# Kernel tuning notes

Hardware: AMD Instinct MI355X
Metric: run time of the kernel (lower is better)

Reference implementation:

```python
import jax, jax.numpy as jnp
import numpy as np

B, C, H, W = 256, 768, 14, 14
S = 196  # sample_size
HID = 512
OUT = 2


def setup_inputs() -> dict:
    key = jax.random.key(0)
    ks = jax.random.split(key, 10)
    x = jax.random.normal(ks[0], (B, C, H, W), dtype=jnp.float32)
    pxs = jax.random.randint(ks[1], (B, S, 2), 0, H, dtype=jnp.int32)
    pys = jax.random.randint(ks[2], (B, S, 2), 0, H, dtype=jnp.int32)
    scale = 0.02
    W1 = jax.random.normal(ks[3], (2 * C, HID), dtype=jnp.float32) * scale
    b1 = jnp.zeros((HID,), dtype=jnp.float32)
    W2 = jax.random.normal(ks[4], (HID, HID), dtype=jnp.float32) * scale
    b2 = jnp.zeros((HID,), dtype=jnp.float32)
    W3 = jax.random.normal(ks[5], (HID, OUT), dtype=jnp.float32) * scale
    b3 = jnp.zeros((OUT,), dtype=jnp.float32)
    return {"x": x, "W1": W1, "b1": b1, "W2": W2, "b2": b2,
            "W3": W3, "b3": b3, "pxs": pxs, "pys": pys}


def _gather_pts(x_flat, pxy):
    # x_flat: [B, C, H*W]; pxy: [B, S, 2] -> [B, S, C]
    idx = pxy[:, :, 0] * W + pxy[:, :, 1]            # [B, S]
    g = jnp.take_along_axis(x_flat, idx[:, None, :].astype(jnp.int32), axis=2)  # [B, C, S]
    return g.transpose(0, 2, 1)                       # [B, S, C]


def reference(x, W1, b1, W2, b2, W3, b3, pxs, pys):
    x_flat = x.reshape(B, C, H * W)
    ptsx = _gather_pts(x_flat, pxs)                   # [B, S, C]
    ptsy = _gather_pts(x_flat, pys)                   # [B, S, C]
    feats = jnp.concatenate([ptsx, ptsy], axis=2)     # [B, S, 2C]
    h = jax.nn.relu(feats @ W1 + b1)
    h = jax.nn.relu(h @ W2 + b2)
    pred = h @ W3 + b3                                # [B, S, 2]
    predxy = pred.reshape(-1, OUT)                    # [B*S, 2]
    # use_abs=False, normalize=False: deltaxy = (pxs - pys) + (H - 1)
    deltaxy = (pxs - pys).astype(jnp.float32).reshape(-1, 2) + (H - 1)
    return predxy, deltaxy
```

## Files before the change

kernel.cpp:

```cpp
#include <hip/hip_runtime.h>
#include <hip/hip_bf16.h>

typedef __attribute__((ext_vector_type(4))) float f32x4;
typedef __attribute__((ext_vector_type(4))) int   int4v;
typedef __attribute__((ext_vector_type(8))) int   int8v;

__device__ __forceinline__ unsigned char f2fp8(float f) {
    unsigned char s = (__float_as_uint(f) >> 24) & 0x80;
    float a = fabsf(f);
    if (a >= 448.f) return s | 0x7E;
    if (a < 0.015625f) {
        int q = (int)(a * 512.0f + 0.5f);
        return s | (unsigned char)q;
    }
    unsigned int u = __float_as_uint(a);
    u += 0x0007FFFF + ((u >> 20) & 1);
    int e8 = (int)((u >> 23) & 0xFF) - 120;
    if (e8 >= 16) return s | 0x7E;
    return s | (unsigned char)((e8 << 3) | ((u >> 20) & 7));
}
__device__ __forceinline__ void gload_lds16(const void* g, void* l) {
    __builtin_amdgcn_global_load_lds((const __attribute__((address_space(1))) void*)g,
                                     (__attribute__((address_space(3))) void*)l, 16, 0, 0);
}

#define BATCH 256
#define CHAN  768
#define HW    196
#define SPS   196
#define HID   512
#define MROWS 50176
#define K1    1536
#define WSCL  64.0f
#define WINV  0.015625f
#define SC1   0x7F7F7F7F


__global__ void transpose_cast_fp8(const float* __restrict__ in, unsigned char* __restrict__ out,
                                   int K, int N) {
    int idx = blockIdx.x * 256 + threadIdx.x;
    if (idx >= K * N) return;
    int n = idx / K, k = idx - n * K;
    out[idx] = f2fp8(in[(size_t)k * N + n] * WSCL);
}

__global__ __launch_bounds__(256) void gather_feats(const float* __restrict__ x,
                                                    const int* __restrict__ pxs,
                                                    const int* __restrict__ pys,
                                                    unsigned char* __restrict__ feats,
                                                    float* __restrict__ out) {
    __shared__ float lds[64 * 197];
    int chunk = blockIdx.x;
    int b     = blockIdx.y;
    int c0 = chunk * 64;
    const float* xb = x + ((size_t)b * CHAN + c0) * HW;
    for (int t = threadIdx.x; t < 64 * HW; t += 256) {
        int j = t / HW, p = t - j * HW;
        lds[j * 197 + p] = xb[t];
    }
    if (chunk == 0) {
        for (int i = threadIdx.x; i < SPS * 2; i += 256) {
            int idx = b * SPS * 2 + i;
            out[MROWS * 2 + idx] = (float)(pxs[idx] - pys[idx]) + 13.0f;
        }
    }
    __syncthreads();
    int wid = threadIdx.x >> 6, lane = threadIdx.x & 63;
    int g = lane >> 4;
    int cq = (lane & 15) * 4;
    for (int sb = wid * 4; sb < SPS; sb += 16) {
        int s = sb + g;
        int base = (b * SPS + s) * 2;
        int ix = pxs[base] * 14 + pxs[base + 1];
        int iy = pys[base] * 14 + pys[base + 1];
        const float* lx = lds + cq * 197;
        unsigned int ux = 0, uy = 0;
        ux = __builtin_amdgcn_cvt_pk_fp8_f32(lx[ix],       lx[197 + ix], ux, false);
        ux = __builtin_amdgcn_cvt_pk_fp8_f32(lx[394 + ix], lx[591 + ix], ux, true);
        uy = __builtin_amdgcn_cvt_pk_fp8_f32(lx[iy],       lx[197 + iy], uy, false);
        uy = __builtin_amdgcn_cvt_pk_fp8_f32(lx[394 + iy], lx[591 + iy], uy, true);
        size_t ro = (size_t)(b * SPS + s) * K1;
        *(unsigned int*)(feats + ro + c0 + cq)        = ux;
        *(unsigned int*)(feats + ro + CHAN + c0 + cq) = uy;
    }
}

__global__ __launch_bounds__(512, 1)
void mlp_fused(const unsigned char* __restrict__ feats,
               const unsigned char* __restrict__ W1t,
               const float* __restrict__ b1,
               const unsigned char* __restrict__ W2t,
               const float* __restrict__ b2,
               const float* __restrict__ W3,
               const float* __restrict__ b3,
               float* __restrict__ out) {
    extern __shared__ char smem[];
    const int t = threadIdx.x;
    const int wid = t >> 6, lane = t & 63;
    const int lr = lane & 15, lk = lane >> 4;
    const int mBase = blockIdx.x * 64;
    f32x4 acc[4][4] = {};

    auto stage1 = [&](int buf, int kt) {
        char* Ab = smem + buf * 8192;
        char* Bb = smem + 16384 + buf * 65536;
        {
            int row = t >> 3, cs = (t & 7) ^ (row & 7);
            gload_lds16(feats + (size_t)(mBase + row) * K1 + kt * 128 + cs * 16,
                        Ab + t * 16);
        }
        #pragma unroll
        for (int i = 0; i < 8; ++i) {
            int lin = i * 512 + t, row = lin >> 3, cs = (lin & 7) ^ (row & 7);
            gload_lds16(W1t + (size_t)row * K1 + kt * 128 + cs * 16,
                        Bb + lin * 16);
        }
    };
    auto frag128 = [&](const char* rowp, int r) -> int8v {
        union { int4v h[2]; int8v v; } u;
        u.h[0] = *(const int4v*)(rowp + (((2 * lk + 0) ^ (r & 7)) * 16));
        u.h[1] = *(const int4v*)(rowp + (((2 * lk + 1) ^ (r & 7)) * 16));
        return u.v;
    };
    auto compute1 = [&](int buf) {
        const char* Ab = smem + buf * 8192;
        const char* Bb = smem + 16384 + buf * 65536;
        int8v af[4];
        #pragma unroll
        for (int m = 0; m < 4; ++m) {
            int r = m * 16 + lr;
            af[m] = frag128(Ab + r * 128, r);
        }
        #pragma unroll
        for (int n = 0; n < 4; ++n) {
            int r = wid * 64 + n * 16 + lr;
            int8v bf = frag128(Bb + r * 128, r);
            #pragma unroll
            for (int m = 0; m < 4; ++m)
                acc[m][n] = __builtin_amdgcn_mfma_scale_f32_16x16x128_f8f6f4(
                    af[m], bf, acc[m][n], 0, 0, 0, SC1, 0, SC1);
        }
    };

    stage1(0, 0);
    __syncthreads();
    int cur = 0;
    for (int kt = 0; kt < 12; ++kt) {
        if (kt + 1 < 12) stage1(cur ^ 1, kt + 1);
        compute1(cur);
        __syncthreads();
        cur ^= 1;
    }

    char* h1l = smem + 16384;
    float* red = (float*)smem;
    #pragma unroll
    for (int n = 0; n < 4; ++n) {
        int c = wid * 64 + n * 16 + lr;
        int c16 = wid * 4 + n;
        float bv = b1[c];
        #pragma unroll
        for (int m = 0; m < 4; ++m) {
            int r0 = m * 16 + lk * 4;
            float v0 = fmaxf(acc[m][n][0] * WINV + bv, 0.f);
            float v1 = fmaxf(acc[m][n][1] * WINV + bv, 0.f);
            float v2 = fmaxf(acc[m][n][2] * WINV + bv, 0.f);
            float v3 = fmaxf(acc[m][n][3] * WINV + bv, 0.f);
            unsigned int u = __builtin_amdgcn_cvt_pk_fp8_f32(v0, v1, 0u, false);
            u = __builtin_amdgcn_cvt_pk_fp8_f32(v2, v3, u, true);
            #pragma unroll
            for (int j = 0; j < 4; ++j) {
                int r = r0 + j;
                h1l[r * 512 + ((c16 ^ (r & 31)) * 16) + lr] =
                    (unsigned char)((u >> (8 * j)) & 0xff);
            }
        }
    }
    __syncthreads();

    auto frag512 = [&](int r, int kt2) -> int8v {
        int g = kt2 * 8 + lk * 2;
        union { int4v h[2]; int8v v; } u;
        u.h[0] = *(const int4v*)(h1l + r * 512 + (((g + 0) ^ (r & 31)) * 16));
        u.h[1] = *(const int4v*)(h1l + r * 512 + (((g + 1) ^ (r & 31)) * 16));
        return u.v;
    };
    #pragma unroll
    for (int p2 = 0; p2 < 2; ++p2) {
        int8v b2f[2][4];
        float bv2[2], w30[2], w31[2];
        #pragma unroll
        for (int n2 = 0; n2 < 2; ++n2) {
            int c2 = wid * 64 + p2 * 32 + n2 * 16 + lr;
            const unsigned char* rp = W2t + (size_t)c2 * 512;
            #pragma unroll
            for (int kt2 = 0; kt2 < 4; ++kt2)
                b2f[n2][kt2] = *(const int8v*)(rp + kt2 * 128 + lk * 32);
            bv2[n2] = b2[c2];
            w30[n2] = W3[c2 * 2];
            w31[n2] = W3[c2 * 2 + 1];
        }
        #pragma unroll
        for (int s = 0; s < 4; ++s) {
            f32x4 acc2[2] = {};
            #pragma unroll
            for (int kt2 = 0; kt2 < 4; ++kt2) {
                int8v a2 = frag512(s * 16 + lr, kt2);
                acc2[0] = __builtin_amdgcn_mfma_scale_f32_16x16x128_f8f6f4(
                    a2, b2f[0][kt2], acc2[0], 0, 0, 0, SC1, 0, SC1);
                acc2[1] = __builtin_amdgcn_mfma_scale_f32_16x16x128_f8f6f4(
                    a2, b2f[1][kt2], acc2[1], 0, 0, 0, SC1, 0, SC1);
            }
            float p0[4] = {0.f, 0.f, 0.f, 0.f}, p1[4] = {0.f, 0.f, 0.f, 0.f};
            #pragma unroll
            for (int n2 = 0; n2 < 2; ++n2) {
                #pragma unroll
                for (int j = 0; j < 4; ++j) {
                    float v = fmaxf(acc2[n2][j] * WINV + bv2[n2], 0.f);
                    p0[j] += v * w30[n2];
                    p1[j] += v * w31[n2];
                }
            }
            #pragma unroll
            for (int j = 0; j < 4; ++j) {
                #pragma unroll
                for (int msk = 1; msk < 16; msk <<= 1) {
                    p0[j] += __shfl_xor(p0[j], msk);
                    p1[j] += __shfl_xor(p1[j], msk);
                }
                if (lr == 0) {
                    int r = s * 16 + lk * 4 + j;
                    if (p2 == 0) {
                        red[r * 17 + wid * 2 + 0] = p0[j];
                        red[r * 17 + wid * 2 + 1] = p1[j];
                    } else {
                        red[r * 17 + wid * 2 + 0] += p0[j];
                        red[r * 17 + wid * 2 + 1] += p1[j];
                    }
                }
            }
        }
    }
    __syncthreads();

    if (t < 128) {
        int row = t >> 1, comp = t & 1;
        float v = b3[comp];
        #pragma unroll
        for (int w = 0; w < 8; ++w)
            v += red[row * 17 + w * 2 + comp];
        out[(size_t)(mBase + row) * 2 + comp] = v;
    }
}

extern "C" void kernel_launch(void* const* d_in, const int* in_sizes, int n_in,
                              void* d_out, int out_size, void* d_ws, size_t ws_size,
                              hipStream_t stream) {
    const float* x  = (const float*)d_in[0];
    const float* W1 = (const float*)d_in[1];
    const float* b1 = (const float*)d_in[2];
    const float* W2 = (const float*)d_in[3];
    const float* b2 = (const float*)d_in[4];
    const float* W3 = (const float*)d_in[5];
    const float* b3 = (const float*)d_in[6];
    const int*  pxs = (const int*)d_in[7];
    const int*  pys = (const int*)d_in[8];
    float* out = (float*)d_out;
    char* ws = (char*)d_ws;

    unsigned char* W1t   = (unsigned char*)(ws + 0);
    unsigned char* W2t   = (unsigned char*)(ws + 786432);
    unsigned char* feats = (unsigned char*)(ws + 1048576);

    hipFuncSetAttribute((const void*)mlp_fused,
                        hipFuncAttributeMaxDynamicSharedMemorySize, 147456);

    transpose_cast_fp8<<<(K1 * HID + 255) / 256, 256, 0, stream>>>(W1, W1t, K1, HID);
    transpose_cast_fp8<<<(HID * HID + 255) / 256, 256, 0, stream>>>(W2, W2t, HID, HID);
    gather_feats<<<dim3(12, BATCH), 256, 0, stream>>>(x, pxs, pys, feats, out);
    mlp_fused<<<MROWS / 64, 512, 147456, stream>>>(feats, W1t, b1, W2t, b2, W3, b3, out);
}
```

Measured before the change: 179.5 us.

## Gather rows inside GEMM from transposed fp8 x, split N into halves

Stops materialising the per-sample feature matrix. x is instead transposed to a pixel-major fp8 layout, and the GEMM loads A tiles by gathered row index, using precomputed pixel indices. The first GEMM is split into two N-halves, which halves the B staging buffer and shared memory and allows two blocks per CU. The two weight-cast kernels are merged into one launch. The risks are recomputing A loads for each half, more register pressure from holding h1 in registers, and scattered row reads.

```diff
diff --git a/kernel.cpp b/kernel.cpp
--- a/kernel.cpp
+++ b/kernel.cpp
@@ -34,145 +34,178 @@
 #define WSCL  64.0f
 #define WINV  0.015625f
 #define SC1   0x7F7F7F7F
-
-
-__global__ void transpose_cast_fp8(const float* __restrict__ in, unsigned char* __restrict__ out,
-                                   int K, int N) {
+#define GPITCH 198
+
+
+__global__ void prep_weights(const float* __restrict__ W1, const float* __restrict__ W2,
+                             unsigned char* __restrict__ W1t, unsigned char* __restrict__ W2t) {
     int idx = blockIdx.x * 256 + threadIdx.x;
-    if (idx >= K * N) return;
-    int n = idx / K, k = idx - n * K;
-    out[idx] = f2fp8(in[(size_t)k * N + n] * WSCL);
-}
-
-__global__ __launch_bounds__(256) void gather_feats(const float* __restrict__ x,
-                                                    const int* __restrict__ pxs,
-                                                    const int* __restrict__ pys,
-                                                    unsigned char* __restrict__ feats,
-                                                    float* __restrict__ out) {
-    __shared__ float lds[64 * 197];
+    if (idx < K1 * HID) {
+        int n = idx / K1, k = idx - n * K1;
+        W1t[idx] = f2fp8(W1[(size_t)k * HID + n] * WSCL);
+    } else {
+        int i = idx - K1 * HID;
+        int n = i / HID, k = i - n * HID;
+        W2t[i] = f2fp8(W2[(size_t)k * HID + n] * WSCL);
+    }
+}
+
+__global__ __launch_bounds__(512) void xpose8(const float* __restrict__ x,
+                                              const int* __restrict__ pxs,
+                                              const int* __restrict__ pys,
+                                              unsigned char* __restrict__ x8,
+                                              int* __restrict__ pidx,
+                                              float* __restrict__ out) {
+    __shared__ float lds[64 * GPITCH];
     int chunk = blockIdx.x;
     int b     = blockIdx.y;
     int c0 = chunk * 64;
-    const float* xb = x + ((size_t)b * CHAN + c0) * HW;
-    for (int t = threadIdx.x; t < 64 * HW; t += 256) {
-        int j = t / HW, p = t - j * HW;
-        lds[j * 197 + p] = xb[t];
+    const float4* xb4 = (const float4*)(x + ((size_t)b * CHAN + c0) * HW);
+    for (int vt = threadIdx.x; vt < 64 * 49; vt += 512) {
+        float4 v = xb4[vt];
+        int j = vt / 49, p4 = vt - j * 49;
+        float* dst = &lds[j * GPITCH + p4 * 4];
+        *(float2*)(dst + 0) = make_float2(v.x, v.y);
+        *(float2*)(dst + 2) = make_float2(v.z, v.w);
     }
     if (chunk == 0) {
-        for (int i = threadIdx.x; i < SPS * 2; i += 256) {
+        for (int i = threadIdx.x; i < SPS * 2; i += 512) {
             int idx = b * SPS * 2 + i;
             out[MROWS * 2 + idx] = (float)(pxs[idx] - pys[idx]) + 13.0f;
+        }
+        for (int s = threadIdx.x; s < SPS; s += 512) {
+            int base = (b * SPS + s) * 2;
+            int ix = pxs[base] * 14 + pxs[base + 1];
+            int iy = pys[base] * 14 + pys[base + 1];
+            pidx[(b * SPS + s) * 2 + 0] = b * HW + ix;
+            pidx[(b * SPS + s) * 2 + 1] = b * HW + iy;
         }
     }
     __syncthreads();
     int wid = threadIdx.x >> 6, lane = threadIdx.x & 63;
     int g = lane >> 4;
     int cq = (lane & 15) * 4;
-    for (int sb = wid * 4; sb < SPS; sb += 16) {
-        int s = sb + g;
-        int base = (b * SPS + s) * 2;
-        int ix = pxs[base] * 14 + pxs[base + 1];
-        int iy = pys[base] * 14 + pys[base + 1];
-        const float* lx = lds + cq * 197;
-        unsigned int ux = 0, uy = 0;
-        ux = __builtin_amdgcn_cvt_pk_fp8_f32(lx[ix],       lx[197 + ix], ux, false);
-        ux = __builtin_amdgcn_cvt_pk_fp8_f32(lx[394 + ix], lx[591 + ix], ux, true);
-        uy = __builtin_amdgcn_cvt_pk_fp8_f32(lx[iy],       lx[197 + iy], uy, false);
-        uy = __builtin_amdgcn_cvt_pk_fp8_f32(lx[394 + iy], lx[591 + iy], uy, true);
-        size_t ro = (size_t)(b * SPS + s) * K1;
-        *(unsigned int*)(feats + ro + c0 + cq)        = ux;
-        *(unsigned int*)(feats + ro + CHAN + c0 + cq) = uy;
-    }
-}
-
-__global__ __launch_bounds__(512, 1)
-void mlp_fused(const unsigned char* __restrict__ feats,
+    const float* lx = lds + cq * GPITCH;
+    for (int pb = wid * 4; pb < HW; pb += 32) {
+        int p = pb + g;
+        unsigned int u = 0;
+        u = __builtin_amdgcn_cvt_pk_fp8_f32(lx[p],              lx[GPITCH + p],     u, false);
+        u = __builtin_amdgcn_cvt_pk_fp8_f32(lx[2 * GPITCH + p], lx[3 * GPITCH + p], u, true);
+        *(unsigned int*)(x8 + ((size_t)b * HW + p) * CHAN + c0 + cq) = u;
+    }
+}
+
+__global__ __launch_bounds__(512, 2)
+void gemm_full(const unsigned char* __restrict__ x8,
                const unsigned char* __restrict__ W1t,
                const float* __restrict__ b1,
                const unsigned char* __restrict__ W2t,
                const float* __restrict__ b2,
                const float* __restrict__ W3,
                const float* __restrict__ b3,
+               const int* __restrict__ pidx,
                float* __restrict__ out) {
     extern __shared__ char smem[];
     const int t = threadIdx.x;
     const int wid = t >> 6, lane = t & 63;
     const int lr = lane & 15, lk = lane >> 4;
     const int mBase = blockIdx.x * 64;
-    f32x4 acc[4][4] = {};
-
-    auto stage1 = [&](int buf, int kt) {
-        char* Ab = smem + buf * 8192;
-        char* Bb = smem + 16384 + buf * 65536;
-        {
-            int row = t >> 3, cs = (t & 7) ^ (row & 7);
-            gload_lds16(feats + (size_t)(mBase + row) * K1 + kt * 128 + cs * 16,
-                        Ab + t * 16);
-        }
-        #pragma unroll
-        for (int i = 0; i < 8; ++i) {
-            int lin = i * 512 + t, row = lin >> 3, cs = (lin & 7) ^ (row & 7);
-            gload_lds16(W1t + (size_t)row * K1 + kt * 128 + cs * 16,
-                        Bb + lin * 16);
-        }
-    };
+    const int gr = mBase + (t >> 3);
+    const int prx = pidx[gr * 2 + 0];
+    const int pry = pidx[gr * 2 + 1];
+
     auto frag128 = [&](const char* rowp, int r) -> int8v {
         union { int4v h[2]; int8v v; } u;
         u.h[0] = *(const int4v*)(rowp + (((2 * lk + 0) ^ (r & 7)) * 16));
         u.h[1] = *(const int4v*)(rowp + (((2 * lk + 1) ^ (r & 7)) * 16));
         return u.v;
     };
-    auto compute1 = [&](int buf) {
-        const char* Ab = smem + buf * 8192;
-        const char* Bb = smem + 16384 + buf * 65536;
-        int8v af[4];
-        #pragma unroll
-        for (int m = 0; m < 4; ++m) {
-            int r = m * 16 + lr;
-            af[m] = frag128(Ab + r * 128, r);
-        }
-        #pragma unroll
-        for (int n = 0; n < 4; ++n) {
-            int r = wid * 64 + n * 16 + lr;
-            int8v bf = frag128(Bb + r * 128, r);
-            #pragma unroll
-            for (int m = 0; m < 4; ++m)
-                acc[m][n] = __builtin_amdgcn_mfma_scale_f32_16x16x128_f8f6f4(
-                    af[m], bf, acc[m][n], 0, 0, 0, SC1, 0, SC1);
-        }
-    };
-
-    stage1(0, 0);
-    __syncthreads();
-    int cur = 0;
-    for (int kt = 0; kt < 12; ++kt) {
-        if (kt + 1 < 12) stage1(cur ^ 1, kt + 1);
-        compute1(cur);
+
+    unsigned int h1u[2][2][4];
+
+    #pragma unroll
+    for (int half = 0; half < 2; ++half) {
+        const int nBase = half * 256;
+        f32x4 acc[4][2] = {};
+        auto stage = [&](int buf, int kt) {
+            char* Ab = smem + buf * 8192;
+            char* Bb = smem + 16384 + buf * 32768;
+            {
+                int row = t >> 3, cs = (t & 7) ^ (row & 7);
+                int srcRow = (kt < 6) ? prx : pry;
+                int kk = (kt < 6) ? kt : kt - 6;
+                gload_lds16(x8 + (size_t)srcRow * CHAN + kk * 128 + cs * 16,
+                            Ab + t * 16);
+                (void)row;
+            }
+            #pragma unroll
+            for (int i = 0; i < 4; ++i) {
+                int lin = i * 512 + t, row = lin >> 3, cs = (lin & 7) ^ (row & 7);
+                gload_lds16(W1t + (size_t)(nBase + row) * K1 + kt * 128 + cs * 16,
+                            Bb + lin * 16);
+            }
+        };
+        auto compute = [&](int buf) {
+            const char* Ab = smem + buf * 8192;
+            const char* Bb = smem + 16384 + buf * 32768;
+            int8v af[4];
+            #pragma unroll
+            for (int m = 0; m < 4; ++m) {
+                int r = m * 16 + lr;
+                af[m] = frag128(Ab + r * 128, r);
+            }
+            #pragma unroll
+            for (int n = 0; n < 2; ++n) {
+                int r = wid * 32 + n * 16 + lr;
+                int8v bf = frag128(Bb + r * 128, r);
+                #pragma unroll
+                for (int m = 0; m < 4; ++m)
+                    acc[m][n] = __builtin_amdgcn_mfma_scale_f32_16x16x128_f8f6f4(
+                        af[m], bf, acc[m][n], 0, 0, 0, SC1, 0, SC1);
+            }
+        };
+
+        stage(0, 0);
         __syncthreads();
-        cur ^= 1;
-    }
-
-    char* h1l = smem + 16384;
-    float* red = (float*)smem;
+        int cur = 0;
+        for (int kt = 0; kt < 12; ++kt) {
+            if (kt + 1 < 12) stage(cur ^ 1, kt + 1);
+            compute(cur);
+            __syncthreads();
+            cur ^= 1;
+        }
+        #pragma unroll
+        for (int n = 0; n < 2; ++n) {
+            float bv = b1[nBase + wid * 32 + n * 16 + lr];
+            #pragma unroll
+            for (int m = 0; m < 4; ++m) {
+                float v0 = fmaxf(acc[m][n][0] * WINV + bv, 0.f);
+                float v1 = fmaxf(acc[m][n][1] * WINV + bv, 0.f);
+                float v2 = fmaxf(acc[m][n][2] * WINV + bv, 0.f);
+                float v3 = fmaxf(acc[m][n][3] * WINV + bv, 0.f);
+                unsigned int u = __builtin_amdgcn_cvt_pk_fp8_f32(v0, v1, 0u, false);
+                u = __builtin_amdgcn_cvt_pk_fp8_f32(v2, v3, u, true);
+                h1u[half][n][m] = u;
+            }
+        }
+    }
+
+    char* h1l = smem;
+    float* red = (float*)(smem + 32768);
     #pragma unroll
-    for (int n = 0; n < 4; ++n) {
-        int c = wid * 64 + n * 16 + lr;
-        int c16 = wid * 4 + n;
-        float bv = b1[c];
-        #pragma unroll
-        for (int m = 0; m < 4; ++m) {
-            int r0 = m * 16 + lk * 4;
-            float v0 = fmaxf(acc[m][n][0] * WINV + bv, 0.f);
-            float v1 = fmaxf(acc[m][n][1] * WINV + bv, 0.f);
-            float v2 = fmaxf(acc[m][n][2] * WINV + bv, 0.f);
-            float v3 = fmaxf(acc[m][n][3] * WINV + bv, 0.f);
-            unsigned int u = __builtin_amdgcn_cvt_pk_fp8_f32(v0, v1, 0u, false);
-            u = __builtin_amdgcn_cvt_pk_fp8_f32(v2, v3, u, true);
-            #pragma unroll
-            for (int j = 0; j < 4; ++j) {
-                int r = r0 + j;
-                h1l[r * 512 + ((c16 ^ (r & 31)) * 16) + lr] =
-                    (unsigned char)((u >> (8 * j)) & 0xff);
+    for (int half = 0; half < 2; ++half) {
+        #pragma unroll
+        for (int n = 0; n < 2; ++n) {
+            int cc = half * 16 + wid * 2 + n;
+            #pragma unroll
+            for (int m = 0; m < 4; ++m) {
+                unsigned int u = h1u[half][n][m];
+                #pragma unroll
+                for (int j = 0; j < 4; ++j) {
+                    int r = m * 16 + lk * 4 + j;
+                    h1l[r * 512 + ((cc ^ (r & 31)) * 16) + lr] =
+                        (unsigned char)((u >> (8 * j)) & 0xff);
+                }
             }
         }
     }
@@ -191,7 +224,7 @@
         float bv2[2], w30[2], w31[2];
         #pragma unroll
         for (int n2 = 0; n2 < 2; ++n2) {
-            int c2 = wid * 64 + p2 * 32 + n2 * 16 + lr;
+            int c2 = p2 * 256 + wid * 32 + n2 * 16 + lr;
             const unsigned char* rp = W2t + (size_t)c2 * 512;
             #pragma unroll
             for (int kt2 = 0; kt2 < 4; ++kt2)
@@ -268,15 +301,15 @@
     float* out = (float*)d_out;
     char* ws = (char*)d_ws;
 
-    unsigned char* W1t   = (unsigned char*)(ws + 0);
-    unsigned char* W2t   = (unsigned char*)(ws + 786432);
-    unsigned char* feats = (unsigned char*)(ws + 1048576);
-
-    hipFuncSetAttribute((const void*)mlp_fused,
-                        hipFuncAttributeMaxDynamicSharedMemorySize, 147456);
-
-    transpose_cast_fp8<<<(K1 * HID + 255) / 256, 256, 0, stream>>>(W1, W1t, K1, HID);
-    transpose_cast_fp8<<<(HID * HID + 255) / 256, 256, 0, stream>>>(W2, W2t, HID, HID);
-    gather_feats<<<dim3(12, BATCH), 256, 0, stream>>>(x, pxs, pys, feats, out);
-    mlp_fused<<<MROWS / 64, 512, 147456, stream>>>(feats, W1t, b1, W2t, b2, W3, b3, out);
-}
+    unsigned char* W1t  = (unsigned char*)(ws + 0);
+    unsigned char* W2t  = (unsigned char*)(ws + 786432);
+    unsigned char* x8   = (unsigned char*)(ws + 1048576);
+    int*           pidx = (int*)(ws + 39583744);
+
+    hipFuncSetAttribute((const void*)gemm_full,
+                        hipFuncAttributeMaxDynamicSharedMemorySize, 81920);
+
+    prep_weights<<<(K1 * HID + HID * HID) / 256, 256, 0, stream>>>(W1, W2, W1t, W2t);
+    xpose8<<<dim3(12, BATCH), 512, 0, stream>>>(x, pxs, pys, x8, pidx, out);
+    gemm_full<<<MROWS / 64, 512, 81920, stream>>>(x8, W1t, b1, W2t, b2, W3, b3, pidx, out);
+}
```

Result: slower. 184.8 us (+2.9%).
